# Optimization experiments

Hardware: AMD Instinct MI355X
Metric: run time of the kernel (lower is better)

Reference implementation:

```python
import jax, jax.numpy as jnp
import numpy as np

N_LAYERS = 2
D = 128


def _prelu(z, a):
    return jnp.where(z >= 0, z, a * z)


def _seg_sum(vals, idx, num):
    return jax.ops.segment_sum(vals, idx, num_segments=num)


def _conv_layer(x, ni, ei, Wn2e, bn2e, We2n, be2n, alpha, Dn_inv, De_inv, num_nodes, num_edges):
    # node -> edge: mean over member nodes (row norm), then linear + bias + PReLU
    e = _seg_sum((x @ Wn2e)[ni] * De_inv[ei][:, None], ei, num_edges) + bn2e
    e = _prelu(e, alpha)
    # edge -> node: mean over incident hyperedges
    n = _seg_sum((e @ We2n)[ei] * Dn_inv[ni][:, None], ni, num_nodes) + be2n
    return n, e


def _encoder(x, ni, ei, Wn2e, bn2e, We2n, be2n, alpha, Dn_inv, De_inv, num_nodes, num_edges):
    e = None
    for i in range(N_LAYERS):
        x, e = _conv_layer(x, ni, ei, Wn2e[i], bn2e[i], We2n[i], be2n[i], alpha, Dn_inv, De_inv, num_nodes, num_edges)
        x = _prelu(x, alpha)
    return x, e


def _decoder(x, e, ni, ei, We, Wx, b, alpha, Dn_inv, num_nodes):
    for i in range(N_LAYERS):
        m = _seg_sum((e @ We[i])[ei] * Dn_inv[ni][:, None], ni, num_nodes)
        x = _prelu(x @ Wx[i] + m + b[i], alpha)
    return x


def _forward(x, xx,
             e1_Wn2e, e1_bn2e, e1_We2n, e1_be2n,
             e2_Wn2e, e2_bn2e, e2_We2n, e2_be2n,
             d1_We, d1_Wx, d1_b, d2_We, d2_Wx, d2_b,
             alpha, node_idx, edge_idx, num_nodes, num_edges):
    # self loops: each node gets its own private hyperedge (id num_edges + node_id)
    ni = jnp.concatenate([node_idx, jnp.arange(num_nodes, dtype=node_idx.dtype)])
    ei = jnp.concatenate([edge_idx, jnp.arange(num_edges, num_edges + num_nodes, dtype=edge_idx.dtype)])
    ne_tot = num_edges + num_nodes
    ones = jnp.ones(ni.shape[0], x.dtype)
    Dn = _seg_sum(ones, ni, num_nodes)
    De = _seg_sum(ones, ei, ne_tot)
    Dn_inv = jnp.where(Dn > 0, 1.0 / Dn, 0.0)
    De_inv = jnp.where(De > 0, 1.0 / De, 0.0)

    n1, e1 = _encoder(x, ni, ei, e1_Wn2e, e1_bn2e, e1_We2n, e1_be2n, alpha, Dn_inv, De_inv, num_nodes, ne_tot)
    n2, e2 = _encoder(xx, ni, ei, e2_Wn2e, e2_bn2e, e2_We2n, e2_be2n, alpha, Dn_inv, De_inv, num_nodes, ne_tot)

    x11 = _decoder(n1, e1, ni, ei, d1_We, d1_Wx, d1_b, alpha, Dn_inv, num_nodes)
    x21 = _decoder(n2, e2, ni, ei, d2_We, d2_Wx, d2_b, alpha, Dn_inv, num_nodes)
    x12 = _decoder(n2, e2, ni, ei, d1_We, d1_Wx, d1_b, alpha, Dn_inv, num_nodes)
    x22 = _decoder(n1, e1, ni, ei, d2_We, d2_Wx, d2_b, alpha, Dn_inv, num_nodes)

    nn1 = jnp.concatenate([n1, n2], axis=1)
    return (nn1, n1, e1[:num_edges], n2, e2[:num_edges], x11, x21, x12, x22)


def setup_inputs() -> dict:
    key = jax.random.key(0)
    ks = jax.random.split(key, 24)
    N, E, NNZ = 50000, 20000, 800000
    s = 1.0 / np.sqrt(D)
    inp = {
        'x': jax.random.normal(ks[0], (N, D), jnp.float32),
        'xx': jax.random.normal(ks[1], (N, D), jnp.float32),
        'node_idx': jax.random.randint(ks[2], (NNZ,), 0, N, jnp.int32),
        'edge_idx': jax.random.randint(ks[3], (NNZ,), 0, E, jnp.int32),
        'num_nodes': N,
        'num_edges': E,
        'alpha': jnp.float32(0.25),
    }
    i = 4
    for enc in ('e1', 'e2'):
        inp[enc + '_Wn2e'] = jax.random.normal(ks[i], (N_LAYERS, D, D), jnp.float32) * s; i += 1
        inp[enc + '_bn2e'] = jnp.zeros((N_LAYERS, D), jnp.float32)
        inp[enc + '_We2n'] = jax.random.normal(ks[i], (N_LAYERS, D, D), jnp.float32) * s; i += 1
        inp[enc + '_be2n'] = jnp.zeros((N_LAYERS, D), jnp.float32)
    for dec in ('d1', 'd2'):
        inp[dec + '_We'] = jax.random.normal(ks[i], (N_LAYERS, D, D), jnp.float32) * s; i += 1
        inp[dec + '_Wx'] = jax.random.normal(ks[i], (N_LAYERS, D, D), jnp.float32) * s; i += 1
        inp[dec + '_b'] = jnp.zeros((N_LAYERS, D), jnp.float32)
    return inp


def reference(x, xx,
              e1_Wn2e, e1_bn2e, e1_We2n, e1_be2n,
              e2_Wn2e, e2_bn2e, e2_We2n, e2_be2n,
              d1_We, d1_Wx, d1_b, d2_We, d2_Wx, d2_b,
              alpha, node_idx, edge_idx, num_nodes, num_edges):
    return _forward(x, xx,
                    e1_Wn2e, e1_bn2e, e1_We2n, e1_be2n,
                    e2_Wn2e, e2_bn2e, e2_We2n, e2_be2n,
                    d1_We, d1_Wx, d1_b, d2_We, d2_Wx, d2_b,
                    alpha, node_idx, edge_idx, num_nodes, num_edges)
```

## Files before the change

### kernel.cpp

```cpp
#include <hip/hip_runtime.h>

#define DD 128

typedef __attribute__((ext_vector_type(8))) short bh8;
typedef __attribute__((ext_vector_type(8))) unsigned short us8;
typedef __attribute__((ext_vector_type(4))) unsigned short us4;
typedef __attribute__((ext_vector_type(4))) float f4;
typedef unsigned int u32;
typedef unsigned short u16;

__device__ __forceinline__ u16 tob(float f) {
  u32 u = __builtin_bit_cast(u32, f);
  u += 0x7FFFu + ((u >> 16) & 1u);
  return (u16)(u >> 16);
}
__device__ __forceinline__ float fb(u16 h) { return __builtin_bit_cast(float, (u32)h << 16); }


__global__ __launch_bounds__(256) void init_counts_k(int* cn, int* ce, int N, int E) {
  int g = blockIdx.x * blockDim.x + threadIdx.x;
  if (g < E) ce[g] = 0;
  if (g < N) cn[g] = 0;
}


__global__ __launch_bounds__(256) void scan_partials_k(const int* __restrict__ cn, const int* __restrict__ ce,
                                                       int* part, int NCHN, int N, int NCHE, int E) {
  __shared__ int red[256];
  int b = blockIdx.x, tid = threadIdx.x;
  const int* cnt = (b < NCHN) ? cn : ce;
  int n = (b < NCHN) ? N : E;
  int base = ((b < NCHN) ? b : (b - NCHN)) << 10;
  int i0 = base + tid * 4;
  int s = 0;
  #pragma unroll
  for (int j = 0; j < 4; ++j) { int i = i0 + j; if (i < n) s += cnt[i]; }
  red[tid] = s; __syncthreads();
  for (int off = 128; off > 0; off >>= 1) {
    if (tid < off) red[tid] += red[tid + off];
    __syncthreads();
  }
  if (tid == 0) part[b] = red[0];
}

__device__ __forceinline__ int blk_excl_scan(int s, int tid, int* sums) {
  sums[tid] = s; __syncthreads();
  for (int off = 1; off < 256; off <<= 1) {
    int t = (tid >= off) ? sums[tid - off] : 0;
    __syncthreads();
    sums[tid] += t;
    __syncthreads();
  }
  int ex = sums[tid] - s;
  __syncthreads();
  return ex;
}

__global__ __launch_bounds__(256) void scan_chunks_k(int* part, int NCHN, int NCHE) {
  __shared__ int sums[256];
  int tid = threadIdx.x;
  {
    int v = (tid < NCHN) ? part[tid] : 0;
    int ex = blk_excl_scan(v, tid, sums);
    if (tid < NCHN) part[tid] = ex;
  }
  __syncthreads();
  {
    int v = (tid < NCHE) ? part[NCHN + tid] : 0;
    int ex = blk_excl_scan(v, tid, sums);
    if (tid < NCHE) part[NCHN + tid] = ex;
  }
}

__global__ __launch_bounds__(256) void scan_apply_k(const int* __restrict__ cn, const int* __restrict__ ce,
                                                    const int* __restrict__ part,
                                                    int* offs_n, int* offs_e,
                                                    int NCHN, int N, int NCHE, int E) {
  __shared__ int sums[256];
  int b = blockIdx.x, tid = threadIdx.x;
  const int* cnt = (b < NCHN) ? cn : ce;
  int* offs = (b < NCHN) ? offs_n : offs_e;
  int n = (b < NCHN) ? N : E;
  int base = ((b < NCHN) ? b : (b - NCHN)) << 10;
  int i0 = base + tid * 4;
  int v[4]; int s = 0;
  #pragma unroll
  for (int j = 0; j < 4; ++j) { int i = i0 + j; int t = (i < n) ? cnt[i] : 0; v[j] = t; s += t; }
  int ex = blk_excl_scan(s, tid, sums);
  int run = part[b] + ex;
  #pragma unroll
  for (int j = 0; j < 4; ++j) { int i = i0 + j; if (i < n) offs[i] = run; run += v[j]; }
  if (tid == 255 && base + 1024 >= n) offs[n] = run;
}

__global__ __launch_bounds__(256) void fill_deg_k(const int* __restrict__ offs_n, const int* __restrict__ offs_e,
                                                  float* Dn_inv, float* De_inv,
                                                  int* cur_be, int* cur_bn, int* cur_n, int* cur_e,
                                                  int N, int E, int NBE, int NBN) {
  int g = blockIdx.x * blockDim.x + threadIdx.x;
  if (g < E) {
    int b = offs_e[g], e = offs_e[g + 1];
    De_inv[g] = (e > b) ? 1.0f / (float)(e - b) : 0.0f;
    cur_e[g] = b;
  }
  if (g < N) {
    int b = offs_n[g], e = offs_n[g + 1];
    Dn_inv[g] = 1.0f / (float)(e - b + 1);
    cur_n[g] = b;
  }
  if (g < NBE) {
    int r1 = (g + 1) * 32; if (r1 > E) r1 = E;
    int o0 = offs_e[g * 32], o1 = offs_e[r1];
    int C = o1 - o0, base = 8 * o0;
    #pragma unroll
    for (int k = 0; k < 8; ++k) cur_be[g * 8 + k] = base + k * C;
  }
  if (g < NBN) {
    int r1 = (g + 1) * 32; if (r1 > N) r1 = N;
    int o0 = offs_n[g * 32], o1 = offs_n[r1];
    int C = o1 - o0, base = 8 * o0;
    #pragma unroll
    for (int k = 0; k < 8; ++k) cur_bn[g * 8 + k] = base + k * C;
  }
}

__global__ __launch_bounds__(256) void partition2_k(const int* __restrict__ ni, const int* __restrict__ ei,
                                                    int* cur_be, int* cur_bn,
                                                    u32* __restrict__ SE, u32* __restrict__ SN, int nnz) {
  int xcd;
  asm volatile("s_getreg_b32 %0, hwreg(HW_REG_XCC_ID)" : "=s"(xcd));
  xcd &= 7;
  int stride = gridDim.x * blockDim.x;
  for (int j = blockIdx.x * blockDim.x + threadIdx.x; j < nnz; j += stride) {
    int n = ni[j], e = ei[j];
    int pe = atomicAdd(&cur_be[(e >> 5) * 8 + xcd], 1);
    SE[pe] = ((u32)(e & 31) << 17) | (u32)n;
    int pn = atomicAdd(&cur_bn[(n >> 5) * 8 + xcd], 1);
    SN[pn] = ((u32)(n & 31) << 17) | (u32)e;
  }
}

__device__ __forceinline__ void scatter_body(const u32* __restrict__ S, const int* __restrict__ offs,
                                             const int* __restrict__ cur_b,
                                             int* __restrict__ list, int nRows, int b, int tid, int* cur) {
  const int i0 = b << 5;
  if (tid < 32) {
    int row = i0 + tid;
    cur[tid] = (row < nRows) ? offs[row] : 0;
  }
  __syncthreads();
  int r1 = i0 + 32; if (r1 > nRows) r1 = nRows;
  const int o0 = offs[i0];
  const int C = offs[r1] - o0;
  #pragma unroll 1
  for (int k = 0; k < 8; ++k) {
    int sbeg = 8 * o0 + k * C;
    int send = cur_b[b * 8 + k];
    for (int i = sbeg + tid; i < send; i += 256) {
      u32 v = S[i];
      int pos = atomicAdd(&cur[v >> 17], 1);
      list[pos] = (int)(v & 0x1FFFFu);
    }
  }
}

__global__ __launch_bounds__(256) void scatter_both_k(const u32* SE, const int* offs_e, const int* cur_be,
                                                      int* listE, int E, int NBE,
                                                      const u32* SN, const int* offs_n, const int* cur_bn,
                                                      int* listN, int N) {
  __shared__ int cur[32];
  int b = blockIdx.x, tid = threadIdx.x;
  if (b < NBE) scatter_body(SE, offs_e, cur_be, listE, E, b, tid, cur);
  else         scatter_body(SN, offs_n, cur_bn, listN, N, b - NBE, tid, cur);
}


__device__ __forceinline__ void acc8(float a[8], us8 v) {
  #pragma unroll
  for (int j = 0; j < 8; ++j) a[j] += fb(v[j]);
}

template<int SPLIT>
__global__ __launch_bounds__(256) void gather_edge_k(const u16* __restrict__ srcb,
                                                     const int* __restrict__ offs, const int* __restrict__ list,
                                                     const float* __restrict__ De_inv,
                                                     const float* __restrict__ b1, const float* __restrict__ b2,
                                                     const float* __restrict__ alphap,
                                                     u16* __restrict__ e_fullb,
                                                     float* __restrict__ d2a, float* __restrict__ d2b, int E) {
  const int wave = threadIdx.x >> 6, lane = threadIdx.x & 63;
  const int row = blockIdx.x * 4 + wave;
  if (row >= E) return;
  const int half = lane >> 5, cl = lane & 31;
  const int c8 = cl * 8;
  const int beg = offs[row], end = offs[row + 1];
  float a0[8] = {0,0,0,0,0,0,0,0}, a1[8] = {0,0,0,0,0,0,0,0};
  int i = beg + half;
  for (; i + 2 < end; i += 4) {
    us8 v0 = *(const us8*)&srcb[(size_t)list[i] * 256 + c8];
    us8 v1 = *(const us8*)&srcb[(size_t)list[i + 2] * 256 + c8];
    acc8(a0, v0); acc8(a1, v1);
  }
  if (i < end) acc8(a0, *(const us8*)&srcb[(size_t)list[i] * 256 + c8]);
  float s[8];
  #pragma unroll
  for (int j = 0; j < 8; ++j) s[j] = a0[j] + a1[j];
  #pragma unroll
  for (int j = 0; j < 8; ++j) s[j] += __shfl_xor(s[j], 32);
  if (half == 0) {
    float sc = De_inv[row];
    const float* bp = (c8 < 128) ? (b1 + c8) : (b2 + c8 - 128);
    float4 bt0 = *(const float4*)bp;
    float4 bt1 = *(const float4*)(bp + 4);
    float bb[8] = {bt0.x, bt0.y, bt0.z, bt0.w, bt1.x, bt1.y, bt1.z, bt1.w};
    float al = *alphap;
    us8 ob;
    float ov[8];
    #pragma unroll
    for (int j = 0; j < 8; ++j) {
      float v = sc * s[j] + bb[j];
      v = (v >= 0.f) ? v : al * v;
      ov[j] = v; ob[j] = tob(v);
    }
    *(us8*)&e_fullb[(size_t)row * 256 + c8] = ob;
    if constexpr (SPLIT == 1) {
      float* dp = (c8 < 128) ? &d2a[(size_t)row * DD + c8] : &d2b[(size_t)row * DD + c8 - 128];
      float4 w0 = {ov[0], ov[1], ov[2], ov[3]};
      float4 w1 = {ov[4], ov[5], ov[6], ov[7]};
      *(float4*)dp = w0;
      *(float4*)(dp + 4) = w1;
    }
  }
}

__global__ __launch_bounds__(256) void gather_node_k(const u16* __restrict__ e_fullb,
                                                     const u16* __restrict__ tb,
                                                     const int* __restrict__ offs, const int* __restrict__ list,
                                                     const float* __restrict__ Dn_inv,
                                                     const float* __restrict__ b1, const float* __restrict__ b2,
                                                     const float* __restrict__ alphap,
                                                     u16* __restrict__ dstb, int N) {
  const int wave = threadIdx.x >> 6, lane = threadIdx.x & 63;
  const int row = blockIdx.x * 4 + wave;
  if (row >= N) return;
  const int half = lane >> 5, cl = lane & 31;
  const int c8 = cl * 8;
  const int beg = offs[row], end = offs[row + 1];
  float a0[8] = {0,0,0,0,0,0,0,0}, a1[8] = {0,0,0,0,0,0,0,0};
  int i = beg + half;
  for (; i + 2 < end; i += 4) {
    us8 v0 = *(const us8*)&e_fullb[(size_t)list[i] * 256 + c8];
    us8 v1 = *(const us8*)&e_fullb[(size_t)list[i + 2] * 256 + c8];
    acc8(a0, v0); acc8(a1, v1);
  }
  if (i < end) acc8(a0, *(const us8*)&e_fullb[(size_t)list[i] * 256 + c8]);
  float s[8];
  #pragma unroll
  for (int j = 0; j < 8; ++j) s[j] = a0[j] + a1[j];
  #pragma unroll
  for (int j = 0; j < 8; ++j) s[j] += __shfl_xor(s[j], 32);
  if (half == 0) {
    us8 tv = *(const us8*)&tb[(size_t)row * 256 + c8];
    const float* bp = (c8 < 128) ? (b1 + c8) : (b2 + c8 - 128);
    float4 bt0 = *(const float4*)bp;
    float4 bt1 = *(const float4*)(bp + 4);
    float bb[8] = {bt0.x, bt0.y, bt0.z, bt0.w, bt1.x, bt1.y, bt1.z, bt1.w};
    float al = *alphap;
    float sc = Dn_inv[row];
    us8 ob;
    #pragma unroll
    for (int j = 0; j < 8; ++j) {
      float sv = fb(tv[j]) + bb[j];
      sv = (sv >= 0.f) ? sv : al * sv;
      ob[j] = tob(sc * (sv + s[j]));
    }
    *(us8*)&dstb[(size_t)row * 256 + c8] = ob;
  }
}


struct WPtrs { const float* p[16]; };

__global__ __launch_bounds__(256) void prep_w_k(WPtrs wp, char* dst) {
  int m = blockIdx.x >> 3, s = blockIdx.x & 7;
  const float* W = wp.p[m];
  int t = threadIdx.x;
  int n = t & 127;
  int k0 = s * 16 + (t >> 7) * 8;
  us8 vhi, vlo;
  #pragma unroll
  for (int j = 0; j < 8; ++j) {
    float x = W[(size_t)(k0 + j) * DD + n];
    u32 ux = __builtin_bit_cast(u32, x);
    float hf = __builtin_bit_cast(float, ux & 0xFFFF0000u);
    float l = x - hf;
    vhi[j] = (u16)(ux >> 16);
    vlo[j] = (u16)(__builtin_bit_cast(u32, l) >> 16);
  }
  char* base = dst + (size_t)m * 65536;
  int byte = n * 256 + k0 * 2;
  byte ^= (n & 7) << 4;
  *(us8*)(base + byte) = vhi;
  *(us8*)(base + 32768 + byte) = vlo;
}


__device__ __forceinline__ void stage_w(const char* gsrc, char* lds, int tid) {
  int wave = tid >> 6, lane = tid & 63;
  #pragma unroll
  for (int i = 0; i < 16; ++i) {
    int off = (wave * 16 + i) * 1024;
    __builtin_amdgcn_global_load_lds(
        (const __attribute__((address_space(1))) u32*)(gsrc + off + lane * 16),
        (__attribute__((address_space(3))) u32*)(lds + off), 16, 0, 0);
  }
}

__device__ __forceinline__ void split8(const float vs[8], bh8& hi, bh8& lo) {
  #pragma unroll
  for (int j = 0; j < 8; ++j) {
    u32 u = __builtin_bit_cast(u32, vs[j]);
    float hf = __builtin_bit_cast(float, u & 0xFFFF0000u);
    float l = vs[j] - hf;
    hi[j] = (short)(u >> 16);
    lo[j] = (short)(__builtin_bit_cast(u32, l) >> 16);
  }
}

__device__ __forceinline__ void mk_afrag(const float* rowp, int koff, bh8& hi, bh8& lo) {
  float4 v0 = *(const float4*)(rowp + koff);
  float4 v1 = *(const float4*)(rowp + koff + 4);
  float vs[8] = {v0.x, v0.y, v0.z, v0.w, v1.x, v1.y, v1.z, v1.w};
  split8(vs, hi, lo);
}

__device__ __forceinline__ void mfma_ks(const bh8& ahi, const bh8& alo, const char* Wl,
                                        int ks, int lane, f4 acc[8]) {
  const int koff0 = (lane >> 4) * 8;
  const int k2 = (ks * 32 + koff0) * 2;
  #pragma unroll
  for (int cb = 0; cb < 8; ++cb) {
    int n = cb * 16 + (lane & 15);
    int byte = (n * 256 + k2) ^ ((n & 7) << 4);
    bh8 bhiF = *(const bh8*)(Wl + byte);
    bh8 bloF = *(const bh8*)(Wl + 32768 + byte);
    acc[cb] = __builtin_amdgcn_mfma_f32_16x16x32_bf16(ahi, bhiF, acc[cb], 0, 0, 0);
    acc[cb] = __builtin_amdgcn_mfma_f32_16x16x32_bf16(ahi, bloF, acc[cb], 0, 0, 0);
    acc[cb] = __builtin_amdgcn_mfma_f32_16x16x32_bf16(alo, bhiF, acc[cb], 0, 0, 0);
  }
}

__device__ __forceinline__ void mfma_ks_bf(const bh8& a, const char* Wl,
                                           int ks, int lane, f4 acc[8]) {
  const int koff0 = (lane >> 4) * 8;
  const int k2 = (ks * 32 + koff0) * 2;
  #pragma unroll
  for (int cb = 0; cb < 8; ++cb) {
    int n = cb * 16 + (lane & 15);
    int byte = (n * 256 + k2) ^ ((n & 7) << 4);
    bh8 bhiF = *(const bh8*)(Wl + byte);
    bh8 bloF = *(const bh8*)(Wl + 32768 + byte);
    acc[cb] = __builtin_amdgcn_mfma_f32_16x16x32_bf16(a, bhiF, acc[cb], 0, 0, 0);
    acc[cb] = __builtin_amdgcn_mfma_f32_16x16x32_bf16(a, bloF, acc[cb], 0, 0, 0);
  }
}

__device__ __forceinline__ void mfma_passS(const float* __restrict__ A, size_t astride, int acoff,
                                           const char* Wl, int rbase, int nrows, int lane, f4 acc[8]) {
  int r = rbase + (lane & 15);
  if (r >= nrows) r = nrows - 1;
  const float* rowp = A + (size_t)r * astride + acoff;
  const int koff0 = (lane >> 4) * 8;
  #pragma unroll
  for (int ks = 0; ks < 4; ++ks) {
    bh8 ahi, alo;
    mk_afrag(rowp, ks * 32 + koff0, ahi, alo);
    mfma_ks(ahi, alo, Wl, ks, lane, acc);
  }
}

__device__ __forceinline__ void mfma_passB(const u16* __restrict__ A, size_t astride, int acoff,
                                           const char* Wl, int rbase, int nrows, int lane, f4 acc[8]) {
  int r = rbase + (lane & 15);
  if (r >= nrows) r = nrows - 1;
  const u16* rowp = A + (size_t)r * astride + acoff;
  const int koff0 = (lane >> 4) * 8;
  #pragma unroll
  for (int ks = 0; ks < 4; ++ks) {
    bh8 a = __builtin_bit_cast(bh8, *(const us8*)(rowp + ks * 32 + koff0));
    mfma_ks_bf(a, Wl, ks, lane, acc);
  }
}

struct AFragB { bh8 a[4]; };

__device__ __forceinline__ void load_afragB(const u16* __restrict__ A, size_t astride, int acoff,
                                            int rbase, int nrows, int lane, AFragB& f) {
  int r = rbase + (lane & 15);
  if (r >= nrows) r = nrows - 1;
  const u16* rowp = A + (size_t)r * astride + acoff;
  const int koff0 = (lane >> 4) * 8;
  #pragma unroll
  for (int ks = 0; ks < 4; ++ks)
    f.a[ks] = __builtin_bit_cast(bh8, *(const us8*)(rowp + ks * 32 + koff0));
}

__device__ __forceinline__ void mfma_pass_fragB(const AFragB& f, const char* Wl, int lane, f4 acc[8]) {
  #pragma unroll
  for (int ks = 0; ks < 4; ++ks) mfma_ks_bf(f.a[ks], Wl, ks, lane, acc);
}


__device__ __forceinline__ void acc_to_T(f4 acc[8], const float* bias, float al,
                                         char* Tb, int wave, int lane) {
  const int cidx = lane & 15;
  float b8[8];
  #pragma unroll
  for (int cb = 0; cb < 8; ++cb) b8[cb] = bias[cb * 16 + cidx];
  #pragma unroll
  for (int q = 0; q < 4; ++q) {
    int row = wave * 16 + (lane >> 4) * 4 + q;
    #pragma unroll
    for (int cb = 0; cb < 8; ++cb) {
      float v = acc[cb][q] + b8[cb];
      v = (v >= 0.f) ? v : al * v;
      int byte = (row * 256 + (cb * 16 + cidx) * 2) ^ ((row & 7) << 4);
      *(u16*)(Tb + byte) = tob(v);
    }
  }
}

__device__ __forceinline__ void load_fT(const char* Tb, int wave, int lane, AFragB& f) {
  const int row = wave * 16 + (lane & 15);
  const int koff0 = (lane >> 4) * 8;
  #pragma unroll
  for (int ks = 0; ks < 4; ++ks) {
    int byte = (row * 256 + (ks * 32 + koff0) * 2) ^ ((row & 7) << 4);
    f.a[ks] = __builtin_bit_cast(bh8, *(const us8*)(Tb + byte));
  }
}

template<int MODE, int OBF>
__device__ __forceinline__ void epilogueS(f4 acc[8], const float* bias, const float* alphap,
                                          void* outp, size_t ostride, int ocoff,
                                          int rbase, int nrows, int lane) {
  float al = 0.f;
  if constexpr (MODE == 1) al = *alphap;
  const int cidx = lane & 15;
  int rq = rbase + (lane >> 4) * 4;
  float b8[8];
  if constexpr (MODE == 1) {
    #pragma unroll
    for (int cb = 0; cb < 8; ++cb) b8[cb] = bias[cb * 16 + cidx];
  }
  #pragma unroll
  for (int q = 0; q < 4; ++q) {
    int row = rq + q;
    if (row < nrows) {
      #pragma unroll
      for (int cb = 0; cb < 8; ++cb) {
        float v = acc[cb][q];
        if constexpr (MODE == 1) { v += b8[cb]; v = (v >= 0.f) ? v : al * v; }
        if constexpr (OBF == 1) {
          u16* op = (u16*)outp + (size_t)row * ostride + ocoff + cidx;
          op[cb * 16] = tob(v);
        } else {
          float* op = (float*)outp + (size_t)row * ostride + ocoff + cidx;
          op[cb * 16] = v;
        }
      }
    }
  }
}

#define ACC_ZERO(acc) { _Pragma("unroll") for (int cb = 0; cb < 8; ++cb) acc[cb] = {0.f, 0.f, 0.f, 0.f}; }


__global__ __launch_bounds__(256, 2) void combo1_k(const float* __restrict__ x, const char* W0,
                                                   const float* __restrict__ xx, const char* W4,
                                                   u16* __restrict__ tb, int nrows, int NT,
                                                   const int* __restrict__ ni, const int* __restrict__ ei,
                                                   int* cn, int* ce, int nnz) {
  __shared__ char Wl[65536];
  if ((int)blockIdx.x < NT) {
    const int wave = threadIdx.x >> 6, lane = threadIdx.x & 63;
    const int rbase = blockIdx.x * 64 + wave * 16;
    f4 acc[8];
    stage_w(W0, Wl, threadIdx.x);
    __syncthreads();
    ACC_ZERO(acc);
    mfma_passS(x, DD, 0, Wl, rbase, nrows, lane, acc);
    epilogueS<0, 1>(acc, nullptr, nullptr, tb, 256, 0, rbase, nrows, lane);
    __syncthreads();
    stage_w(W4, Wl, threadIdx.x);
    __syncthreads();
    ACC_ZERO(acc);
    mfma_passS(xx, DD, 0, Wl, rbase, nrows, lane, acc);
    epilogueS<0, 1>(acc, nullptr, nullptr, tb, 256, 128, rbase, nrows, lane);
  } else {
    int nb = gridDim.x - NT;
    int stride = nb * 256;
    for (int j = ((int)blockIdx.x - NT) * 256 + (int)threadIdx.x; j < nnz; j += stride) {
      atomicAdd(&cn[ni[j]], 1);
      atomicAdd(&ce[ei[j]], 1);
    }
  }
}

__global__ __launch_bounds__(256, 2) void gemm_fuse_hid_k(const u16* __restrict__ thb,
                                                          const char* W20, const float* b20, const char* W21,
                                                          const char* W60, const float* b60, const char* W61,
                                                          const float* __restrict__ alphap,
                                                          u16* __restrict__ tb_out, int nrows) {
  __shared__ char Wl[65536];
  const int wave = threadIdx.x >> 6, lane = threadIdx.x & 63;
  const int rbase = blockIdx.x * 64 + wave * 16;
  const float al = *alphap;
  f4 acc[8];
  AFragB fT;
  #pragma unroll 1
  for (int h = 0; h < 2; ++h) {
    if (h) __syncthreads();
    stage_w(h ? W60 : W20, Wl, threadIdx.x);
    __syncthreads();
    ACC_ZERO(acc);
    mfma_passB(thb, 256, h * 128, Wl, rbase, nrows, lane, acc);
    __syncthreads();
    acc_to_T(acc, h ? b60 : b20, al, Wl, wave, lane);
    __syncthreads();
    load_fT(Wl, wave, lane, fT);
    __syncthreads();
    stage_w(h ? W61 : W21, Wl, threadIdx.x);
    __syncthreads();
    ACC_ZERO(acc);
    mfma_pass_fragB(fT, Wl, lane, acc);
    epilogueS<0, 1>(acc, nullptr, nullptr, tb_out, 256, h * 128, rbase, nrows, lane);
  }
}

__global__ __launch_bounds__(256, 2) void enc_final_k(const u16* __restrict__ aggb, const char* W1, const float* b1_,
                                                      const char* W2, const float* b2_,
                                                      const float* __restrict__ alphap,
                                                      float* __restrict__ n1, float* __restrict__ n2,
                                                      u16* __restrict__ n1b, u16* __restrict__ n2b,
                                                      float* __restrict__ nn1, int nrows) {
  __shared__ char Wl[65536];
  const int wave = threadIdx.x >> 6, lane = threadIdx.x & 63;
  const int rbase = blockIdx.x * 64 + wave * 16;
  const int cidx = lane & 15;
  f4 acc[8];
  float al = *alphap;
  #pragma unroll 1
  for (int h = 0; h < 2; ++h) {
    if (h) __syncthreads();
    stage_w(h ? W2 : W1, Wl, threadIdx.x);
    __syncthreads();
    const float* bp = h ? b2_ : b1_;
    float* nout = h ? n2 : n1;
    u16* nbout = h ? n2b : n1b;
    float b8[8];
    #pragma unroll
    for (int cb = 0; cb < 8; ++cb) b8[cb] = bp[cb * 16 + cidx];
    ACC_ZERO(acc);
    mfma_passB(aggb, 256, h * 128, Wl, rbase, nrows, lane, acc);
    int rq = rbase + (lane >> 4) * 4;
    #pragma unroll
    for (int q = 0; q < 4; ++q) {
      int row = rq + q;
      if (row < nrows) {
        float* op = nout + (size_t)row * DD + cidx;
        float* op2 = nn1 + (size_t)row * 256 + h * 128 + cidx;
        u16* op3 = nbout + (size_t)row * DD + cidx;
        #pragma unroll
        for (int cb = 0; cb < 8; ++cb) {
          float v = acc[cb][q] + b8[cb];
          v = (v >= 0.f) ? v : al * v;
          op[cb * 16] = v;
          op2[cb * 16] = v;
          op3[cb * 16] = tob(v);
        }
      }
    }
  }
}

__global__ __launch_bounds__(256, 2) void dec_fused_k(const u16* __restrict__ n1b, const u16* __restrict__ n2b,
                                                      const u16* __restrict__ aggb,
                                                      const char* Wx10, const char* We10, const float* b1_0,
                                                      const char* Wx11, const char* We11, const float* b1_1,
                                                      const char* Wx20, const char* We20, const float* b2_0,
                                                      const char* Wx21, const char* We21, const float* b2_1,
                                                      const float* __restrict__ alphap,
                                                      float* __restrict__ x11, float* __restrict__ x22,
                                                      float* __restrict__ x12, float* __restrict__ x21,
                                                      int nrows) {
  __shared__ char Wl[65536];
  const int y = blockIdx.y;
  const u16* xb = y ? n2b : n1b;
  float* od1 = y ? x12 : x11;
  float* od2 = y ? x21 : x22;
  const int acoff = y * 128;
  const int wave = threadIdx.x >> 6, lane = threadIdx.x & 63;
  const int rbase = blockIdx.x * 64 + wave * 16;
  const float al = *alphap;
  AFragB fx, fa, fT;
  load_afragB(xb, DD, 0, rbase, nrows, lane, fx);
  load_afragB(aggb, 256, acoff, rbase, nrows, lane, fa);
  f4 acc[8];
  #pragma unroll 1
  for (int s = 0; s < 2; ++s) {
    const char* Wx0 = s ? Wx20 : Wx10;
    const char* We0 = s ? We20 : We10;
    const char* Wx1 = s ? Wx21 : Wx11;
    const char* We1 = s ? We21 : We11;
    const float* b0 = s ? b2_0 : b1_0;
    const float* b1 = s ? b2_1 : b1_1;
    float* out = s ? od2 : od1;
    if (s) __syncthreads();
    stage_w(Wx0, Wl, threadIdx.x);
    __syncthreads();
    ACC_ZERO(acc);
    mfma_pass_fragB(fx, Wl, lane, acc);
    __syncthreads();
    stage_w(We0, Wl, threadIdx.x);
    __syncthreads();
    mfma_pass_fragB(fa, Wl, lane, acc);
    __syncthreads();
    acc_to_T(acc, b0, al, Wl, wave, lane);
    __syncthreads();
    load_fT(Wl, wave, lane, fT);
    __syncthreads();
    stage_w(Wx1, Wl, threadIdx.x);
    __syncthreads();
    ACC_ZERO(acc);
    mfma_pass_fragB(fT, Wl, lane, acc);
    __syncthreads();
    stage_w(We1, Wl, threadIdx.x);
    __syncthreads();
    mfma_pass_fragB(fa, Wl, lane, acc);
    epilogueS<1, 0>(acc, b1, alphap, out, DD, 0, rbase, nrows, lane);
  }
}


extern "C" void kernel_launch(void* const* d_in, const int* in_sizes, int n_in,
                              void* d_out, int out_size, void* d_ws, size_t ws_size,
                              hipStream_t stream) {
  const float* x        = (const float*)d_in[0];
  const float* xx       = (const float*)d_in[1];
  const int*   node_idx = (const int*)d_in[2];
  const int*   edge_idx = (const int*)d_in[3];
  const float* alphap   = (const float*)d_in[6];
  const float* e1_Wn2e  = (const float*)d_in[7];
  const float* e1_bn2e  = (const float*)d_in[8];
  const float* e1_We2n  = (const float*)d_in[9];
  const float* e1_be2n  = (const float*)d_in[10];
  const float* e2_Wn2e  = (const float*)d_in[11];
  const float* e2_bn2e  = (const float*)d_in[12];
  const float* e2_We2n  = (const float*)d_in[13];
  const float* e2_be2n  = (const float*)d_in[14];
  const float* d1_We    = (const float*)d_in[15];
  const float* d1_Wx    = (const float*)d_in[16];
  const float* d1_b     = (const float*)d_in[17];
  const float* d2_We    = (const float*)d_in[18];
  const float* d2_Wx    = (const float*)d_in[19];
  const float* d2_b     = (const float*)d_in[20];

  const int N   = in_sizes[0] / DD;
  const int NNZ = in_sizes[2];
  const int E   = (out_size - 1024 * N) / 256;
  const int NBE = (E + 31) >> 5;
  const int NBN = (N + 31) >> 5;
  const int NCHN = (N + 1023) >> 10;
  const int NCHE = (E + 1023) >> 10;

  float* out  = (float*)d_out;
  float* nn1  = out;
  float* n1   = out + (size_t)N * 256;
  float* e1o  = n1 + (size_t)N * DD;
  float* n2   = e1o + (size_t)E * DD;
  float* e2o  = n2 + (size_t)N * DD;
  float* x11  = e2o + (size_t)E * DD;
  float* x21  = x11 + (size_t)N * DD;
  float* x12  = x21 + (size_t)N * DD;
  float* x22  = x12 + (size_t)N * DD;

  size_t off = 0;
  char* w0 = (char*)d_ws;
  auto carve = [&](size_t bytes) -> void* {
    void* p = (void*)(w0 + off);
    off += (bytes + 255) & ~(size_t)255;
    return p;
  };
  int* cn      = (int*)carve((size_t)N * 4);
  int* ce      = (int*)carve((size_t)E * 4);
  int* offs_n  = (int*)carve((size_t)(N + 1) * 4);
  int* offs_e  = (int*)carve((size_t)(E + 1) * 4);
  int* part    = (int*)carve((size_t)(NCHN + NCHE) * 4);
  int* listN   = (int*)carve((size_t)NNZ * 4);
  int* listE   = (int*)carve((size_t)NNZ * 4);
  float* Dn_inv = (float*)carve((size_t)N * 4);
  float* De_inv = (float*)carve((size_t)E * 4);
  char* Wprep  = (char*)carve((size_t)16 * 65536);
  u16* tb      = (u16*)carve((size_t)N * 256 * 2);
  u16* e_fullb = (u16*)carve((size_t)E * 256 * 2);
  u16* thb     = (u16*)carve((size_t)N * 256 * 2);
  u16* aggb    = (u16*)carve((size_t)N * 256 * 2);
  u16* n1b     = (u16*)carve((size_t)N * DD * 2);
  u16* n2b     = (u16*)carve((size_t)N * DD * 2);
  int* cur_n   = (int*)carve((size_t)N * 4);
  int* cur_e   = (int*)carve((size_t)E * 4);
  int* cur_be  = (int*)carve((size_t)NBE * 8 * 4);
  int* cur_bn  = (int*)carve((size_t)NBN * 8 * 4);
  u32* SE      = (u32*)carve((size_t)NNZ * 8 * 4);
  u32* SN      = (u32*)carve((size_t)NNZ * 8 * 4);
  (void)cur_n; (void)cur_e;

  WPtrs wp;
  wp.p[0] = e1_Wn2e;  wp.p[1] = e1_Wn2e + DD * DD;
  wp.p[2] = e1_We2n;  wp.p[3] = e1_We2n + DD * DD;
  wp.p[4] = e2_Wn2e;  wp.p[5] = e2_Wn2e + DD * DD;
  wp.p[6] = e2_We2n;  wp.p[7] = e2_We2n + DD * DD;
  wp.p[8] = d1_We;    wp.p[9] = d1_We + DD * DD;
  wp.p[10] = d1_Wx;   wp.p[11] = d1_Wx + DD * DD;
  wp.p[12] = d2_We;   wp.p[13] = d2_We + DD * DD;
  wp.p[14] = d2_Wx;   wp.p[15] = d2_Wx + DD * DD;
  auto WP = [&](int i) -> const char* { return Wprep + (size_t)i * 65536; };

  const int thr = 256;
  const int gMax = ((N > E ? N : E) + thr - 1) / thr;
  const int NT = (N + 63) / 64;
  const int HB = 512;
  int gNNZ = (NNZ + thr - 1) / thr; if (gNNZ > 2048) gNNZ = 2048;
  const int gGatE = (E + 3) / 4;
  const int gGatN = (N + 3) / 4;

  prep_w_k<<<128, 256, 0, stream>>>(wp, Wprep);
  init_counts_k<<<gMax, thr, 0, stream>>>(cn, ce, N, E);
  combo1_k<<<NT + HB, 256, 0, stream>>>(x, WP(0), xx, WP(4), tb, N, NT,
                                        node_idx, edge_idx, cn, ce, NNZ);
  scan_partials_k<<<NCHN + NCHE, 256, 0, stream>>>(cn, ce, part, NCHN, N, NCHE, E);
  scan_chunks_k<<<1, 256, 0, stream>>>(part, NCHN, NCHE);
  scan_apply_k<<<NCHN + NCHE, 256, 0, stream>>>(cn, ce, part, offs_n, offs_e, NCHN, N, NCHE, E);
  fill_deg_k<<<gMax, thr, 0, stream>>>(offs_n, offs_e, Dn_inv, De_inv,
                                       cur_be, cur_bn, cur_n, cur_e, N, E, NBE, NBN);
  partition2_k<<<gNNZ, thr, 0, stream>>>(node_idx, edge_idx, cur_be, cur_bn, SE, SN, NNZ);
  scatter_both_k<<<NBE + NBN, 256, 0, stream>>>(SE, offs_e, cur_be, listE, E, NBE,
                                                SN, offs_n, cur_bn, listN, N);

  gather_edge_k<0><<<gGatE, 256, 0, stream>>>(tb, offs_e, listE, De_inv, e1_bn2e, e2_bn2e,
                                              alphap, e_fullb, nullptr, nullptr, E);
  gather_node_k<<<gGatN, 256, 0, stream>>>(e_fullb, tb, offs_n, listN, Dn_inv, e1_bn2e, e2_bn2e,
                                           alphap, thb, N);
  gemm_fuse_hid_k<<<NT, 256, 0, stream>>>(thb, WP(2), e1_be2n, WP(1),
                                          WP(6), e2_be2n, WP(5), alphap, tb, N);
  gather_edge_k<1><<<gGatE, 256, 0, stream>>>(tb, offs_e, listE, De_inv, e1_bn2e + DD, e2_bn2e + DD,
                                              alphap, e_fullb, e1o, e2o, E);
  gather_node_k<<<gGatN, 256, 0, stream>>>(e_fullb, tb, offs_n, listN, Dn_inv, e1_bn2e + DD, e2_bn2e + DD,
                                           alphap, aggb, N);
  enc_final_k<<<NT, 256, 0, stream>>>(aggb, WP(3), e1_be2n + DD, WP(7), e2_be2n + DD,
                                      alphap, n1, n2, n1b, n2b, nn1, N);

  dim3 gDec(NT, 2);
  dec_fused_k<<<gDec, 256, 0, stream>>>(n1b, n2b, aggb,
                                        WP(10), WP(8), d1_b, WP(11), WP(9), d1_b + DD,
                                        WP(14), WP(12), d2_b, WP(15), WP(13), d2_b + DD,
                                        alphap, x11, x22, x12, x21, N);
}
```

Before: 585.9 us.

## Merge chunk scan into apply, reshape hidden/decoder GEMM grids to 128-row tiles

Removes the single-block scan_chunks kernel: each scan_apply block now rescans the chunk partials itself to find its base offset, saving one launch at the cost of redundant work. gemm_fuse_hid_k and dec_fused_k change from looping over the two encoder/decoder halves inside one block to launching those halves on extra grid dimensions. Each block now processes 128 rows, so every weight staged in LDS is reused twice. Unused cur_n/cur_e writes are also dropped. The trade-off is higher register pressure from the doubled accumulators and fragments.

After: 712.9 us. +21.7%, slower.

```diff
diff --git a/kernel.cpp b/kernel.cpp
--- a/kernel.cpp
+++ b/kernel.cpp
@@ -4,7 +4,6 @@
 
 typedef __attribute__((ext_vector_type(8))) short bh8;
 typedef __attribute__((ext_vector_type(8))) unsigned short us8;
-typedef __attribute__((ext_vector_type(4))) unsigned short us4;
 typedef __attribute__((ext_vector_type(4))) float f4;
 typedef unsigned int u32;
 typedef unsigned short u16;
@@ -56,38 +55,33 @@
   return ex;
 }
 
-__global__ __launch_bounds__(256) void scan_chunks_k(int* part, int NCHN, int NCHE) {
-  __shared__ int sums[256];
-  int tid = threadIdx.x;
-  {
-    int v = (tid < NCHN) ? part[tid] : 0;
-    int ex = blk_excl_scan(v, tid, sums);
-    if (tid < NCHN) part[tid] = ex;
-  }
-  __syncthreads();
-  {
-    int v = (tid < NCHE) ? part[NCHN + tid] : 0;
-    int ex = blk_excl_scan(v, tid, sums);
-    if (tid < NCHE) part[NCHN + tid] = ex;
-  }
-}
-
 __global__ __launch_bounds__(256) void scan_apply_k(const int* __restrict__ cn, const int* __restrict__ ce,
                                                     const int* __restrict__ part,
                                                     int* offs_n, int* offs_e,
                                                     int NCHN, int N, int NCHE, int E) {
   __shared__ int sums[256];
+  __shared__ int base_s;
   int b = blockIdx.x, tid = threadIdx.x;
-  const int* cnt = (b < NCHN) ? cn : ce;
-  int* offs = (b < NCHN) ? offs_n : offs_e;
-  int n = (b < NCHN) ? N : E;
-  int base = ((b < NCHN) ? b : (b - NCHN)) << 10;
+  const bool isN = b < NCHN;
+  const int* cnt = isN ? cn : ce;
+  int* offs = isN ? offs_n : offs_e;
+  int n = isN ? N : E;
+  int nch = isN ? NCHN : NCHE;
+  int c = isN ? b : b - NCHN;
+  const int* pbase = isN ? part : part + NCHN;
+  {
+    int v = (tid < nch) ? pbase[tid] : 0;
+    int ex = blk_excl_scan(v, tid, sums);
+    if (tid == c) base_s = ex;
+  }
+  __syncthreads();
+  int base = (c << 10);
   int i0 = base + tid * 4;
   int v[4]; int s = 0;
   #pragma unroll
   for (int j = 0; j < 4; ++j) { int i = i0 + j; int t = (i < n) ? cnt[i] : 0; v[j] = t; s += t; }
   int ex = blk_excl_scan(s, tid, sums);
-  int run = part[b] + ex;
+  int run = base_s + ex;
   #pragma unroll
   for (int j = 0; j < 4; ++j) { int i = i0 + j; if (i < n) offs[i] = run; run += v[j]; }
   if (tid == 255 && base + 1024 >= n) offs[n] = run;
@@ -95,18 +89,16 @@
 
 __global__ __launch_bounds__(256) void fill_deg_k(const int* __restrict__ offs_n, const int* __restrict__ offs_e,
                                                   float* Dn_inv, float* De_inv,
-                                                  int* cur_be, int* cur_bn, int* cur_n, int* cur_e,
+                                                  int* cur_be, int* cur_bn,
                                                   int N, int E, int NBE, int NBN) {
   int g = blockIdx.x * blockDim.x + threadIdx.x;
   if (g < E) {
     int b = offs_e[g], e = offs_e[g + 1];
     De_inv[g] = (e > b) ? 1.0f / (float)(e - b) : 0.0f;
-    cur_e[g] = b;
   }
   if (g < N) {
     int b = offs_n[g], e = offs_n[g + 1];
     Dn_inv[g] = 1.0f / (float)(e - b + 1);
-    cur_n[g] = b;
   }
   if (g < NBE) {
     int r1 = (g + 1) * 32; if (r1 > E) r1 = E;
@@ -508,34 +500,41 @@
 }
 
 __global__ __launch_bounds__(256, 2) void gemm_fuse_hid_k(const u16* __restrict__ thb,
-                                                          const char* W20, const float* b20, const char* W21,
-                                                          const char* W60, const float* b60, const char* W61,
+                                                          const char* W0a, const float* b0a, const char* W1a,
+                                                          const char* W0b, const float* b0b, const char* W1b,
                                                           const float* __restrict__ alphap,
                                                           u16* __restrict__ tb_out, int nrows) {
   __shared__ char Wl[65536];
+  const int h = blockIdx.y;
+  const char* W0 = h ? W0b : W0a;
+  const char* W1 = h ? W1b : W1a;
+  const float* b0 = h ? b0b : b0a;
   const int wave = threadIdx.x >> 6, lane = threadIdx.x & 63;
-  const int rbase = blockIdx.x * 64 + wave * 16;
+  const int r0 = blockIdx.x * 128 + wave * 16;
+  const int r1 = r0 + 64;
   const float al = *alphap;
-  f4 acc[8];
-  AFragB fT;
-  #pragma unroll 1
-  for (int h = 0; h < 2; ++h) {
-    if (h) __syncthreads();
-    stage_w(h ? W60 : W20, Wl, threadIdx.x);
-    __syncthreads();
-    ACC_ZERO(acc);
-    mfma_passB(thb, 256, h * 128, Wl, rbase, nrows, lane, acc);
-    __syncthreads();
-    acc_to_T(acc, h ? b60 : b20, al, Wl, wave, lane);
-    __syncthreads();
-    load_fT(Wl, wave, lane, fT);
-    __syncthreads();
-    stage_w(h ? W61 : W21, Wl, threadIdx.x);
-    __syncthreads();
-    ACC_ZERO(acc);
-    mfma_pass_fragB(fT, Wl, lane, acc);
-    epilogueS<0, 1>(acc, nullptr, nullptr, tb_out, 256, h * 128, rbase, nrows, lane);
-  }
+  f4 acc0[8], acc1[8];
+  AFragB fT0, fT1;
+  stage_w(W0, Wl, threadIdx.x);
+  __syncthreads();
+  ACC_ZERO(acc0); ACC_ZERO(acc1);
+  mfma_passB(thb, 256, h * 128, Wl, r0, nrows, lane, acc0);
+  mfma_passB(thb, 256, h * 128, Wl, r1, nrows, lane, acc1);
+  __syncthreads();
+  acc_to_T(acc0, b0, al, Wl, wave, lane);
+  acc_to_T(acc1, b0, al, Wl + 16384, wave, lane);
+  __syncthreads();
+  load_fT(Wl, wave, lane, fT0);
+  load_fT(Wl + 16384, wave, lane, fT1);
+  __syncthreads();
+  stage_w(W1, Wl, threadIdx.x);
+  __syncthreads();
+  ACC_ZERO(acc0);
+  mfma_pass_fragB(fT0, Wl, lane, acc0);
+  epilogueS<0, 1>(acc0, nullptr, nullptr, tb_out, 256, h * 128, r0, nrows, lane);
+  ACC_ZERO(acc1);
+  mfma_pass_fragB(fT1, Wl, lane, acc1);
+  epilogueS<0, 1>(acc1, nullptr, nullptr, tb_out, 256, h * 128, r1, nrows, lane);
 }
 
 __global__ __launch_bounds__(256, 2) void enc_final_k(const u16* __restrict__ aggb, const char* W1, const float* b1_,
@@ -586,60 +585,64 @@
 
 __global__ __launch_bounds__(256, 2) void dec_fused_k(const u16* __restrict__ n1b, const u16* __restrict__ n2b,
                                                       const u16* __restrict__ aggb,
-                                                      const char* Wx10, const char* We10, const float* b1_0,
-                                                      const char* Wx11, const char* We11, const float* b1_1,
-                                                      const char* Wx20, const char* We20, const float* b2_0,
-                                                      const char* Wx21, const char* We21, const float* b2_1,
+                                                      const char* Wx1_0, const char* We1_0, const float* b1_0,
+                                                      const char* Wx1_1, const char* We1_1, const float* b1_1,
+                                                      const char* Wx2_0, const char* We2_0, const float* b2_0,
+                                                      const char* Wx2_1, const char* We2_1, const float* b2_1,
                                                       const float* __restrict__ alphap,
                                                       float* __restrict__ x11, float* __restrict__ x22,
                                                       float* __restrict__ x12, float* __restrict__ x21,
                                                       int nrows) {
   __shared__ char Wl[65536];
-  const int y = blockIdx.y;
+  const int y = blockIdx.y, z = blockIdx.z;
   const u16* xb = y ? n2b : n1b;
-  float* od1 = y ? x12 : x11;
-  float* od2 = y ? x21 : x22;
+  float* out = y ? (z ? x21 : x12) : (z ? x22 : x11);
+  const char* Wx0 = z ? Wx2_0 : Wx1_0;
+  const char* We0 = z ? We2_0 : We1_0;
+  const char* Wx1 = z ? Wx2_1 : Wx1_1;
+  const char* We1 = z ? We2_1 : We1_1;
+  const float* b0 = z ? b2_0 : b1_0;
+  const float* b1 = z ? b2_1 : b1_1;
   const int acoff = y * 128;
   const int wave = threadIdx.x >> 6, lane = threadIdx.x & 63;
-  const int rbase = blockIdx.x * 64 + wave * 16;
+  const int r0 = blockIdx.x * 128 + wave * 16;
+  const int r1 = r0 + 64;
   const float al = *alphap;
-  AFragB fx, fa, fT;
-  load_afragB(xb, DD, 0, rbase, nrows, lane, fx);
-  load_afragB(aggb, 256, acoff, rbase, nrows, lane, fa);
-  f4 acc[8];
-  #pragma unroll 1
-  for (int s = 0; s < 2; ++s) {
-    const char* Wx0 = s ? Wx20 : Wx10;
-    const char* We0 = s ? We20 : We10;
-    const char* Wx1 = s ? Wx21 : Wx11;
-    const char* We1 = s ? We21 : We11;
-    const float* b0 = s ? b2_0 : b1_0;
-    const float* b1 = s ? b2_1 : b1_1;
-    float* out = s ? od2 : od1;
-    if (s) __syncthreads();
-    stage_w(Wx0, Wl, threadIdx.x);
-    __syncthreads();
-    ACC_ZERO(acc);
-    mfma_pass_fragB(fx, Wl, lane, acc);
-    __syncthreads();
-    stage_w(We0, Wl, threadIdx.x);
-    __syncthreads();
-    mfma_pass_fragB(fa, Wl, lane, acc);
-    __syncthreads();
-    acc_to_T(acc, b0, al, Wl, wave, lane);
-    __syncthreads();
-    load_fT(Wl, wave, lane, fT);
-    __syncthreads();
-    stage_w(Wx1, Wl, threadIdx.x);
-    __syncthreads();
-    ACC_ZERO(acc);
-    mfma_pass_fragB(fT, Wl, lane, acc);
-    __syncthreads();
-    stage_w(We1, Wl, threadIdx.x);
-    __syncthreads();
-    mfma_pass_fragB(fa, Wl, lane, acc);
-    epilogueS<1, 0>(acc, b1, alphap, out, DD, 0, rbase, nrows, lane);
-  }
+  AFragB fx0, fx1, fa0, fa1, fT0, fT1;
+  load_afragB(xb, DD, 0, r0, nrows, lane, fx0);
+  load_afragB(xb, DD, 0, r1, nrows, lane, fx1);
+  load_afragB(aggb, 256, acoff, r0, nrows, lane, fa0);
+  load_afragB(aggb, 256, acoff, r1, nrows, lane, fa1);
+  f4 acc0[8], acc1[8];
+  stage_w(Wx0, Wl, threadIdx.x);
+  __syncthreads();
+  ACC_ZERO(acc0); ACC_ZERO(acc1);
+  mfma_pass_fragB(fx0, Wl, lane, acc0);
+  mfma_pass_fragB(fx1, Wl, lane, acc1);
+  __syncthreads();
+  stage_w(We0, Wl, threadIdx.x);
+  __syncthreads();
+  mfma_pass_fragB(fa0, Wl, lane, acc0);
+  mfma_pass_fragB(fa1, Wl, lane, acc1);
+  __syncthreads();
+  acc_to_T(acc0, b0, al, Wl, wave, lane);
+  acc_to_T(acc1, b0, al, Wl + 16384, wave, lane);
+  __syncthreads();
+  load_fT(Wl, wave, lane, fT0);
+  load_fT(Wl + 16384, wave, lane, fT1);
+  __syncthreads();
+  stage_w(Wx1, Wl, threadIdx.x);
+  __syncthreads();
+  ACC_ZERO(acc0); ACC_ZERO(acc1);
+  mfma_pass_fragB(fT0, Wl, lane, acc0);
+  mfma_pass_fragB(fT1, Wl, lane, acc1);
+  __syncthreads();
+  stage_w(We1, Wl, threadIdx.x);
+  __syncthreads();
+  mfma_pass_fragB(fa0, Wl, lane, acc0);
+  epilogueS<1, 0>(acc0, b1, alphap, out, DD, 0, r0, nrows, lane);
+  mfma_pass_fragB(fa1, Wl, lane, acc1);
+  epilogueS<1, 0>(acc1, b1, alphap, out, DD, 0, r1, nrows, lane);
 }
 
 
@@ -708,13 +711,10 @@
   u16* aggb    = (u16*)carve((size_t)N * 256 * 2);
   u16* n1b     = (u16*)carve((size_t)N * DD * 2);
   u16* n2b     = (u16*)carve((size_t)N * DD * 2);
-  int* cur_n   = (int*)carve((size_t)N * 4);
-  int* cur_e   = (int*)carve((size_t)E * 4);
   int* cur_be  = (int*)carve((size_t)NBE * 8 * 4);
   int* cur_bn  = (int*)carve((size_t)NBN * 8 * 4);
   u32* SE      = (u32*)carve((size_t)NNZ * 8 * 4);
   u32* SN      = (u32*)carve((size_t)NNZ * 8 * 4);
-  (void)cur_n; (void)cur_e;
 
   WPtrs wp;
   wp.p[0] = e1_Wn2e;  wp.p[1] = e1_Wn2e + DD * DD;
@@ -730,6 +730,7 @@
   const int thr = 256;
   const int gMax = ((N > E ? N : E) + thr - 1) / thr;
   const int NT = (N + 63) / 64;
+  const int NT2 = (N + 127) / 128;
   const int HB = 512;
   int gNNZ = (NNZ + thr - 1) / thr; if (gNNZ > 2048) gNNZ = 2048;
   const int gGatE = (E + 3) / 4;
@@ -740,10 +741,9 @@
   combo1_k<<<NT + HB, 256, 0, stream>>>(x, WP(0), xx, WP(4), tb, N, NT,
                                         node_idx, edge_idx, cn, ce, NNZ);
   scan_partials_k<<<NCHN + NCHE, 256, 0, stream>>>(cn, ce, part, NCHN, N, NCHE, E);
-  scan_chunks_k<<<1, 256, 0, stream>>>(part, NCHN, NCHE);
   scan_apply_k<<<NCHN + NCHE, 256, 0, stream>>>(cn, ce, part, offs_n, offs_e, NCHN, N, NCHE, E);
   fill_deg_k<<<gMax, thr, 0, stream>>>(offs_n, offs_e, Dn_inv, De_inv,
-                                       cur_be, cur_bn, cur_n, cur_e, N, E, NBE, NBN);
+                                       cur_be, cur_bn, N, E, NBE, NBN);
   partition2_k<<<gNNZ, thr, 0, stream>>>(node_idx, edge_idx, cur_be, cur_bn, SE, SN, NNZ);
   scatter_both_k<<<NBE + NBN, 256, 0, stream>>>(SE, offs_e, cur_be, listE, E, NBE,
                                                 SN, offs_n, cur_bn, listN, N);
@@ -752,8 +752,9 @@
                                               alphap, e_fullb, nullptr, nullptr, E);
   gather_node_k<<<gGatN, 256, 0, stream>>>(e_fullb, tb, offs_n, listN, Dn_inv, e1_bn2e, e2_bn2e,
                                            alphap, thb, N);
-  gemm_fuse_hid_k<<<NT, 256, 0, stream>>>(thb, WP(2), e1_be2n, WP(1),
-                                          WP(6), e2_be2n, WP(5), alphap, tb, N);
+  dim3 gHid(NT2, 2);
+  gemm_fuse_hid_k<<<gHid, 256, 0, stream>>>(thb, WP(2), e1_be2n, WP(1),
+                                            WP(6), e2_be2n, WP(5), alphap, tb, N);
   gather_edge_k<1><<<gGatE, 256, 0, stream>>>(tb, offs_e, listE, De_inv, e1_bn2e + DD, e2_bn2e + DD,
                                               alphap, e_fullb, e1o, e2o, E);
   gather_node_k<<<gGatN, 256, 0, stream>>>(e_fullb, tb, offs_n, listN, Dn_inv, e1_bn2e + DD, e2_bn2e + DD,
@@ -761,7 +762,7 @@
   enc_final_k<<<NT, 256, 0, stream>>>(aggb, WP(3), e1_be2n + DD, WP(7), e2_be2n + DD,
                                       alphap, n1, n2, n1b, n2b, nn1, N);
 
-  dim3 gDec(NT, 2);
+  dim3 gDec(NT2, 2, 2);
   dec_fused_k<<<gDec, 256, 0, stream>>>(n1b, n2b, aggb,
                                         WP(10), WP(8), d1_b, WP(11), WP(9), d1_b + DD,
                                         WP(14), WP(12), d2_b, WP(15), WP(13), d2_b + DD,
```
